# Kernel tuning notes

Hardware: AMD Instinct MI355X
Metric: run time of the kernel (lower is better)

## Reference

```python
import jax, jax.numpy as jnp
import numpy as np

K = 3          # kernel_size (local window)
PAD = 1        # padding = (K-1)//2 -> 'same' output size
GROUPS = 8
C_OUT = 64


def _unfold3d(x, k):
    """x: [B,C,Dp,Hp,Wp] -> [B,C,D,H,W,kd,kh,kw] sliding windows (stride 1)."""
    B, C, Dp, Hp, Wp = x.shape
    D, H, W = Dp - k + 1, Hp - k + 1, Wp - k + 1
    idx_d = jnp.arange(D)[:, None] + jnp.arange(k)[None, :]
    idx_h = jnp.arange(H)[:, None] + jnp.arange(k)[None, :]
    idx_w = jnp.arange(W)[:, None] + jnp.arange(k)[None, :]
    x = x[:, :, idx_d]              # [B,C,D,kd,Hp,Wp]
    x = x[:, :, :, :, idx_h]        # [B,C,D,kd,H,kh,Wp]
    x = x[:, :, :, :, :, :, idx_w]  # [B,C,D,kd,H,kh,W,kw]
    return jnp.transpose(x, (0, 1, 2, 4, 6, 3, 5, 7))


def setup_inputs() -> dict:
    key = jax.random.key(0)
    ks = jax.random.split(key, 7)
    B, Cin, D, H, W = 1, 64, 16, 64, 64
    c3 = C_OUT // 3                 # 21
    rest = C_OUT - 2 * c3           # 22
    fan_out_scale = np.sqrt(2.0 / C_OUT)  # kaiming_normal fan_out, relu
    x = jax.random.normal(ks[0], (B, Cin, D, H, W), dtype=jnp.float32)
    w_q = jax.random.normal(ks[1], (C_OUT, Cin), dtype=jnp.float32) * fan_out_scale
    w_k = jax.random.normal(ks[2], (C_OUT, Cin), dtype=jnp.float32) * fan_out_scale
    w_v = jax.random.normal(ks[3], (C_OUT, Cin), dtype=jnp.float32) * fan_out_scale
    rel_d = jax.random.normal(ks[4], (c3, 1, 1, 1, K, 1, 1), dtype=jnp.float32)
    rel_h = jax.random.normal(ks[5], (c3, 1, 1, 1, 1, K, 1), dtype=jnp.float32)
    rel_w = jax.random.normal(ks[6], (rest, 1, 1, 1, 1, 1, K), dtype=jnp.float32)
    return {"x": x, "w_q": w_q, "w_k": w_k, "w_v": w_v,
            "rel_d": rel_d, "rel_h": rel_h, "rel_w": rel_w}


def reference(x, w_q, w_k, w_v, rel_d, rel_h, rel_w):
    B, Cin, D, H, W = x.shape
    cg = C_OUT // GROUPS
    c3 = C_OUT // 3
    # 1x1x1 convs (bias=False): plain channel mixing. conv(pad(x)) == pad(conv(x)).
    q = jnp.einsum('oc,bcdhw->bodhw', w_q, x)
    k = jnp.einsum('oc,bcdhw->bodhw', w_k, x)
    v = jnp.einsum('oc,bcdhw->bodhw', w_v, x)
    pad = [(0, 0), (0, 0), (PAD, PAD), (PAD, PAD), (PAD, PAD)]
    k = jnp.pad(k, pad)
    v = jnp.pad(v, pad)
    k_win = _unfold3d(k, K)   # [B,Co,D,H,W,kd,kh,kw]
    v_win = _unfold3d(v, K)
    # split relative position bias across channel thirds
    k_win = jnp.concatenate([
        k_win[:, :c3] + rel_d,
        k_win[:, c3:2 * c3] + rel_h,
        k_win[:, 2 * c3:] + rel_w,
    ], axis=1)
    Kv = K * K * K
    k_win = k_win.reshape(B, GROUPS, cg, D, H, W, Kv)
    v_win = v_win.reshape(B, GROUPS, cg, D, H, W, Kv)
    qg = q.reshape(B, GROUPS, cg, D, H, W, 1)
    attn = jax.nn.softmax(qg * k_win, axis=-1)
    out = jnp.einsum('bncdhwk,bncdhwk->bncdhw', attn, v_win)
    return out.reshape(B, C_OUT, D, H, W)
```

## Files before the change

kernel.cpp:

```cpp
#include <hip/hip_runtime.h>

#define SP    65536
#define DD    16
#define HH    64
#define WW    64
#define CIN   64
#define COUT  64

#define XP    132
#define WP    68


__global__ __launch_bounds__(256) void proj(const float* __restrict__ x,
                                            const float* __restrict__ wq,
                                            const float* __restrict__ wk,
                                            const float* __restrict__ wv,
                                            float* __restrict__ q,
                                            float* __restrict__ k,
                                            float* __restrict__ v) {
    __shared__ float xl[CIN][XP];
    __shared__ float wl[COUT][WP];

    const int t  = threadIdx.x;
    const int p0 = blockIdx.x * 128;
    const int m  = blockIdx.y;

    const float* __restrict__ wsel = (m == 0) ? wq : (m == 1) ? wk : wv;
    float* __restrict__       osel = (m == 0) ? q  : (m == 1) ? k  : v;

#pragma unroll
    for (int i = 0; i < 8; ++i) {
        const int f = t + 256 * i;
        const int c = f >> 5, j = f & 31;
        *(float4*)(&xl[c][j * 4]) = *(const float4*)(x + c * SP + p0 + j * 4);
    }
#pragma unroll
    for (int i = 0; i < 4; ++i) {
        const int f = t + 256 * i;
        const int o = f >> 4, j = f & 15;
        *(float4*)(&wl[o][j * 4]) = *(const float4*)(wsel + o * CIN + j * 4);
    }
    __syncthreads();

    const int og    = t >> 5;
    const int pg    = t & 31;
    const int obase = og * 8;
    const int pbase = pg * 4;

    float acc[8][4] = {};
#pragma unroll 2
    for (int c4 = 0; c4 < CIN / 4; ++c4) {
        float4 w4[8], x4[4];
#pragma unroll
        for (int i = 0; i < 8; ++i)
            w4[i] = *(const float4*)(&wl[obase + i][c4 * 4]);
#pragma unroll
        for (int cc = 0; cc < 4; ++cc)
            x4[cc] = *(const float4*)(&xl[c4 * 4 + cc][pbase]);
#pragma unroll
        for (int i = 0; i < 8; ++i) {
            const float* wf = (const float*)&w4[i];
#pragma unroll
            for (int cc = 0; cc < 4; ++cc) {
                const float* xf = (const float*)&x4[cc];
                const float wv_ = wf[cc];
                acc[i][0] = fmaf(wv_, xf[0], acc[i][0]);
                acc[i][1] = fmaf(wv_, xf[1], acc[i][1]);
                acc[i][2] = fmaf(wv_, xf[2], acc[i][2]);
                acc[i][3] = fmaf(wv_, xf[3], acc[i][3]);
            }
        }
    }

#pragma unroll
    for (int i = 0; i < 8; ++i)
        *(float4*)(osel + (obase + i) * SP + p0 + pbase) =
            make_float4(acc[i][0], acc[i][1], acc[i][2], acc[i][3]);
}

__device__ __forceinline__ float dpp_shr1(float x) {
    return __int_as_float(__builtin_amdgcn_mov_dpp(__float_as_int(x), 0x111, 0xf, 0xf, true));
}
__device__ __forceinline__ float dpp_shl1(float x) {
    return __int_as_float(__builtin_amdgcn_mov_dpp(__float_as_int(x), 0x101, 0xf, 0xf, true));
}

template<int AXIS>
__device__ __forceinline__ void attn_compute(const float* __restrict__ kt,
                                             const float* __restrict__ vt,
                                             const float (&qs)[4][4],
                                             float r0, float r1, float r2,
                                             int wg, int h, int dg,
                                             float (&s)[4][4], float (&a)[4][4]) {
#pragma unroll 1
    for (int m = 0; m < 6; ++m) {
#pragma unroll 1
        for (int kh = 0; kh < 3; ++kh) {
            const int row = (dg * 4 + m) * 10 + (h + kh);
            const float4 km = *(const float4*)(kt + row * 64 + wg * 4);
            const float4 vm = *(const float4*)(vt + row * 64 + wg * 4);
            const float kl = dpp_shr1(km.w), kr = dpp_shl1(km.x);
            const float vl = dpp_shr1(vm.w), vr = dpp_shl1(vm.x);
            const float krow[6] = { kl, km.x, km.y, km.z, km.w, kr };
            const float vrow[6] = { vl, vm.x, vm.y, vm.z, vm.w, vr };

            const float rkh = (kh == 0) ? r0 : (kh == 1) ? r1 : r2;

#pragma unroll
            for (int di = 0; di < 4; ++di) {
                const int kd = m - di;
                if ((unsigned)kd < 3u) {
                    const float rdd = (kd == 0) ? r0 : (kd == 1) ? r1 : r2;
                    const float rr  = (AXIS == 0) ? rdd : (AXIS == 1) ? rkh : 0.f;
#pragma unroll
                    for (int wi = 0; wi < 4; ++wi) {
                        const float qv = qs[di][wi];
#pragma unroll
                        for (int kw = 0; kw < 3; ++kw) {
                            const float rc = (AXIS == 2)
                                           ? ((kw == 0) ? r0 : (kw == 1) ? r1 : r2)
                                           : rr;
                            const float e = __expf(qv * (krow[wi + kw] + rc));
                            s[di][wi] += e;
                            a[di][wi] = fmaf(e, vrow[wi + kw], a[di][wi]);
                        }
                    }
                }
            }
        }
    }
}

__global__ __launch_bounds__(256) void attn(const float* __restrict__ kbuf,
                                            const float* __restrict__ vbuf,
                                            const float* __restrict__ qbuf,
                                            const float* __restrict__ rel_d,
                                            const float* __restrict__ rel_h,
                                            const float* __restrict__ rel_w,
                                            float* __restrict__ out) {
    __shared__ float kt[100 * 64];
    __shared__ float vt[100 * 64];

    const int dt = blockIdx.x;
    const int ht = blockIdx.y;
    const int o  = blockIdx.z;

    const int d0 = dt * 8;
    const int h0 = ht * 8;
    const int t  = threadIdx.x;

    const float* __restrict__ kc = kbuf + o * SP;
    const float* __restrict__ vc = vbuf + o * SP;

#pragma unroll
    for (int i = 0; i < 13; ++i) {
        const int idx = t + 256 * i;
        if (idx < 3200) {
            const bool isv = idx >= 1600;
            const int rem  = isv ? idx - 1600 : idx;
            const int row  = rem >> 4;
            const int j    = rem & 15;
            const int dp   = row / 10;
            const int hp   = row - dp * 10;
            const int dpg  = d0 - 1 + dp;
            const int hpg  = h0 - 1 + hp;
            float4 val = make_float4(0.f, 0.f, 0.f, 0.f);
            if ((unsigned)dpg < (unsigned)DD && (unsigned)hpg < (unsigned)HH) {
                const float* src = (isv ? vc : kc) + (dpg * HH + hpg) * WW + j * 4;
                val = *(const float4*)src;
            }
            *(float4*)((isv ? vt : kt) + row * 64 + j * 4) = val;
        }
    }

    const int wg = t & 15;
    const int h  = (t >> 4) & 7;
    const int dg = t >> 7;

    float qs[4][4];
#pragma unroll
    for (int di = 0; di < 4; ++di) {
        const int dabs = d0 + dg * 4 + di;
        const float4 q4 = *(const float4*)(qbuf + o * SP + (dabs * HH + (h0 + h)) * WW + wg * 4);
        qs[di][0] = q4.x; qs[di][1] = q4.y; qs[di][2] = q4.z; qs[di][3] = q4.w;
    }

    __syncthreads();

    float s[4][4] = {};
    float a[4][4] = {};

    if (o < 21) {
        attn_compute<0>(kt, vt, qs, rel_d[o * 3 + 0], rel_d[o * 3 + 1], rel_d[o * 3 + 2],
                        wg, h, dg, s, a);
    } else if (o < 42) {
        const int b = o - 21;
        attn_compute<1>(kt, vt, qs, rel_h[b * 3 + 0], rel_h[b * 3 + 1], rel_h[b * 3 + 2],
                        wg, h, dg, s, a);
    } else {
        const int b = o - 42;
        attn_compute<2>(kt, vt, qs, rel_w[b * 3 + 0], rel_w[b * 3 + 1], rel_w[b * 3 + 2],
                        wg, h, dg, s, a);
    }

#pragma unroll
    for (int di = 0; di < 4; ++di) {
        const int dabs = d0 + dg * 4 + di;
        float4 ov;
        ov.x = a[di][0] * __builtin_amdgcn_rcpf(s[di][0]);
        ov.y = a[di][1] * __builtin_amdgcn_rcpf(s[di][1]);
        ov.z = a[di][2] * __builtin_amdgcn_rcpf(s[di][2]);
        ov.w = a[di][3] * __builtin_amdgcn_rcpf(s[di][3]);
        *(float4*)(out + o * SP + (dabs * HH + (h0 + h)) * WW + wg * 4) = ov;
    }
}

extern "C" void kernel_launch(void* const* d_in, const int* in_sizes, int n_in,
                              void* d_out, int out_size, void* d_ws, size_t ws_size,
                              hipStream_t stream) {
    const float* x     = (const float*)d_in[0];
    const float* w_q   = (const float*)d_in[1];
    const float* w_k   = (const float*)d_in[2];
    const float* w_v   = (const float*)d_in[3];
    const float* rel_d = (const float*)d_in[4];
    const float* rel_h = (const float*)d_in[5];
    const float* rel_w = (const float*)d_in[6];
    float* out = (float*)d_out;

    float* ws = (float*)d_ws;
    float* q  = ws;
    float* k  = ws + (size_t)COUT * SP;
    float* v  = ws + 2 * (size_t)COUT * SP;

    proj<<<dim3(SP / 128, 3), 256, 0, stream>>>(x, w_q, w_k, w_v, q, k, v);
    attn<<<dim3(2, 8, 64), 256, 0, stream>>>(k, v, q, rel_d, rel_h, rel_w, out);
}
```

Baseline: 131.1 us.

## Halve depth tile per block, fully unroll attention loop, use exp2 with prescaled q

Each attention block now covers 4 depth slices instead of 8, and each thread handles 2 depth outputs instead of 4. This doubles the grid and shrinks the shared tiles to 60 rows, which should raise occupancy and cut registers per thread. The window loop is now fully unrolled, and q is prescaled by log2(e) so the hardware exp2 can replace __expf. The cost is a larger halo fraction (6 rows loaded for every 4 output rows), so more redundant global loads of k and v.

```diff
diff --git a/kernel.cpp b/kernel.cpp
--- a/kernel.cpp
+++ b/kernel.cpp
@@ -9,6 +9,8 @@
 
 #define XP    132
 #define WP    68
+
+#define LOG2E 1.44269504f
 
 
 __global__ __launch_bounds__(256) void proj(const float* __restrict__ x,
@@ -86,19 +88,19 @@
 }
 
 template<int AXIS>
-__device__ __forceinline__ void attn_compute(const float* __restrict__ kt,
-                                             const float* __restrict__ vt,
-                                             const float (&qs)[4][4],
-                                             float r0, float r1, float r2,
-                                             int wg, int h, int dg,
-                                             float (&s)[4][4], float (&a)[4][4]) {
-#pragma unroll 1
-    for (int m = 0; m < 6; ++m) {
-#pragma unroll 1
+__device__ __forceinline__ void attn_tile(const float* __restrict__ kt,
+                                          const float* __restrict__ vt,
+                                          const float (&ql)[2][4],
+                                          float r0, float r1, float r2,
+                                          int wg, int h, int dg,
+                                          float (&s)[2][4], float (&a)[2][4]) {
+#pragma unroll
+    for (int nl = 0; nl < 4; ++nl) {
+#pragma unroll
         for (int kh = 0; kh < 3; ++kh) {
-            const int row = (dg * 4 + m) * 10 + (h + kh);
-            const float4 km = *(const float4*)(kt + row * 64 + wg * 4);
-            const float4 vm = *(const float4*)(vt + row * 64 + wg * 4);
+            const int off = ((dg * 2 + nl) * 10 + h + kh) * 64 + wg * 4;
+            const float4 km = *(const float4*)(kt + off);
+            const float4 vm = *(const float4*)(vt + off);
             const float kl = dpp_shr1(km.w), kr = dpp_shl1(km.x);
             const float vl = dpp_shr1(vm.w), vr = dpp_shl1(vm.x);
             const float krow[6] = { kl, km.x, km.y, km.z, km.w, kr };
@@ -107,20 +109,20 @@
             const float rkh = (kh == 0) ? r0 : (kh == 1) ? r1 : r2;
 
 #pragma unroll
-            for (int di = 0; di < 4; ++di) {
-                const int kd = m - di;
-                if ((unsigned)kd < 3u) {
+            for (int di = 0; di < 2; ++di) {
+                const int kd = nl - di;
+                if (kd >= 0 && kd < 3) {
                     const float rdd = (kd == 0) ? r0 : (kd == 1) ? r1 : r2;
                     const float rr  = (AXIS == 0) ? rdd : (AXIS == 1) ? rkh : 0.f;
 #pragma unroll
                     for (int wi = 0; wi < 4; ++wi) {
-                        const float qv = qs[di][wi];
+                        const float qv = ql[di][wi];
 #pragma unroll
                         for (int kw = 0; kw < 3; ++kw) {
                             const float rc = (AXIS == 2)
                                            ? ((kw == 0) ? r0 : (kw == 1) ? r1 : r2)
                                            : rr;
-                            const float e = __expf(qv * (krow[wi + kw] + rc));
+                            const float e = __builtin_amdgcn_exp2f(qv * (krow[wi + kw] + rc));
                             s[di][wi] += e;
                             a[di][wi] = fmaf(e, vrow[wi + kw], a[di][wi]);
                         }
@@ -138,14 +140,14 @@
                                             const float* __restrict__ rel_h,
                                             const float* __restrict__ rel_w,
                                             float* __restrict__ out) {
-    __shared__ float kt[100 * 64];
-    __shared__ float vt[100 * 64];
+    __shared__ float kt[60 * 64];
+    __shared__ float vt[60 * 64];
 
     const int dt = blockIdx.x;
     const int ht = blockIdx.y;
     const int o  = blockIdx.z;
 
-    const int d0 = dt * 8;
+    const int d0 = dt * 4;
     const int h0 = ht * 8;
     const int t  = threadIdx.x;
 
@@ -153,16 +155,16 @@
     const float* __restrict__ vc = vbuf + o * SP;
 
 #pragma unroll
-    for (int i = 0; i < 13; ++i) {
+    for (int i = 0; i < 8; ++i) {
         const int idx = t + 256 * i;
-        if (idx < 3200) {
-            const bool isv = idx >= 1600;
-            const int rem  = isv ? idx - 1600 : idx;
+        if (idx < 1920) {
+            const bool isv = idx >= 960;
+            const int rem  = isv ? idx - 960 : idx;
             const int row  = rem >> 4;
             const int j    = rem & 15;
-            const int dp   = row / 10;
-            const int hp   = row - dp * 10;
-            const int dpg  = d0 - 1 + dp;
+            const int nn   = row / 10;
+            const int hp   = row - nn * 10;
+            const int dpg  = d0 - 1 + nn;
             const int hpg  = h0 - 1 + hp;
             float4 val = make_float4(0.f, 0.f, 0.f, 0.f);
             if ((unsigned)dpg < (unsigned)DD && (unsigned)hpg < (unsigned)HH) {
@@ -177,35 +179,36 @@
     const int h  = (t >> 4) & 7;
     const int dg = t >> 7;
 
-    float qs[4][4];
-#pragma unroll
-    for (int di = 0; di < 4; ++di) {
-        const int dabs = d0 + dg * 4 + di;
+    float ql[2][4];
+#pragma unroll
+    for (int di = 0; di < 2; ++di) {
+        const int dabs = d0 + dg * 2 + di;
         const float4 q4 = *(const float4*)(qbuf + o * SP + (dabs * HH + (h0 + h)) * WW + wg * 4);
-        qs[di][0] = q4.x; qs[di][1] = q4.y; qs[di][2] = q4.z; qs[di][3] = q4.w;
+        ql[di][0] = q4.x * LOG2E; ql[di][1] = q4.y * LOG2E;
+        ql[di][2] = q4.z * LOG2E; ql[di][3] = q4.w * LOG2E;
     }
 
     __syncthreads();
 
-    float s[4][4] = {};
-    float a[4][4] = {};
+    float s[2][4] = {};
+    float a[2][4] = {};
 
     if (o < 21) {
-        attn_compute<0>(kt, vt, qs, rel_d[o * 3 + 0], rel_d[o * 3 + 1], rel_d[o * 3 + 2],
-                        wg, h, dg, s, a);
+        attn_tile<0>(kt, vt, ql, rel_d[o * 3 + 0], rel_d[o * 3 + 1], rel_d[o * 3 + 2],
+                     wg, h, dg, s, a);
     } else if (o < 42) {
         const int b = o - 21;
-        attn_compute<1>(kt, vt, qs, rel_h[b * 3 + 0], rel_h[b * 3 + 1], rel_h[b * 3 + 2],
-                        wg, h, dg, s, a);
+        attn_tile<1>(kt, vt, ql, rel_h[b * 3 + 0], rel_h[b * 3 + 1], rel_h[b * 3 + 2],
+                     wg, h, dg, s, a);
     } else {
         const int b = o - 42;
-        attn_compute<2>(kt, vt, qs, rel_w[b * 3 + 0], rel_w[b * 3 + 1], rel_w[b * 3 + 2],
-                        wg, h, dg, s, a);
-    }
-
-#pragma unroll
-    for (int di = 0; di < 4; ++di) {
-        const int dabs = d0 + dg * 4 + di;
+        attn_tile<2>(kt, vt, ql, rel_w[b * 3 + 0], rel_w[b * 3 + 1], rel_w[b * 3 + 2],
+                     wg, h, dg, s, a);
+    }
+
+#pragma unroll
+    for (int di = 0; di < 2; ++di) {
+        const int dabs = d0 + dg * 2 + di;
         float4 ov;
         ov.x = a[di][0] * __builtin_amdgcn_rcpf(s[di][0]);
         ov.y = a[di][1] * __builtin_amdgcn_rcpf(s[di][1]);
@@ -233,5 +236,5 @@
     float* v  = ws + 2 * (size_t)COUT * SP;
 
     proj<<<dim3(SP / 128, 3), 256, 0, stream>>>(x, w_q, w_k, w_v, q, k, v);
-    attn<<<dim3(2, 8, 64), 256, 0, stream>>>(k, v, q, rel_d, rel_h, rel_w, out);
-}
+    attn<<<dim3(4, 8, 64), 256, 0, stream>>>(k, v, q, rel_d, rel_h, rel_w, out);
+}
```

New measurement: 125.7 us. 1.04x faster.
